# Kernel optimization log

Hardware: AMD Instinct MI355X
Metric: run time of the kernel (lower is better)

## Reference

```python
import jax, jax.numpy as jnp
import numpy as np

B, L, DM, H, DFF = 4, 2048, 512, 8, 2048
D = DM // H            # head dim = 64
FACTOR = 5
U = min(FACTOR * int(np.ceil(np.log(L))), L)  # 40 sampled keys / top-u queries
EPS = 1e-5


def layer_norm(x, g, b):
    m = x.mean(-1, keepdims=True)
    v = ((x - m) ** 2).mean(-1, keepdims=True)
    return (x - m) * jax.lax.rsqrt(v + EPS) * g + b


def setup_inputs() -> dict:
    key = jax.random.key(0)
    ks = jax.random.split(key, 18)
    s = 0.02  # init scale for stability
    return {
        "x": jax.random.normal(ks[0], (B, L, DM), jnp.float32),
        "Wq": jax.random.normal(ks[1], (DM, DM), jnp.float32) * s,
        "bq": jnp.zeros((DM,), jnp.float32),
        "Wk": jax.random.normal(ks[2], (DM, DM), jnp.float32) * s,
        "bk": jnp.zeros((DM,), jnp.float32),
        "Wv": jax.random.normal(ks[3], (DM, DM), jnp.float32) * s,
        "bv": jnp.zeros((DM,), jnp.float32),
        "Wo": jax.random.normal(ks[4], (DM, DM), jnp.float32) * s,
        "bo": jnp.zeros((DM,), jnp.float32),
        "Wc1": jax.random.normal(ks[5], (DFF, DM), jnp.float32) * s,  # conv1d k=1 weight (out,in)
        "bc1": jnp.zeros((DFF,), jnp.float32),
        "Wc2": jax.random.normal(ks[6], (DM, DFF), jnp.float32) * s,
        "bc2": jnp.zeros((DM,), jnp.float32),
        "ln1_g": jnp.ones((DM,), jnp.float32),
        "ln1_b": jnp.zeros((DM,), jnp.float32),
        "ln2_g": jnp.ones((DM,), jnp.float32),
        "ln2_b": jnp.zeros((DM,), jnp.float32),
        "sample_idx": jax.random.randint(ks[7], (L, U), 0, L, jnp.int32),
    }


def reference(x, Wq, bq, Wk, bk, Wv, bv, Wo, bo, Wc1, bc1, Wc2, bc2,
              ln1_g, ln1_b, ln2_g, ln2_b, sample_idx):
    Bb, Ll, _ = x.shape
    # --- AttentionLayer projections -> (B, H, L, D) ---
    q = (x @ Wq + bq).reshape(Bb, Ll, H, D).transpose(0, 2, 1, 3)
    k = (x @ Wk + bk).reshape(Bb, Ll, H, D).transpose(0, 2, 1, 3)
    v = (x @ Wv + bv).reshape(Bb, Ll, H, D).transpose(0, 2, 1, 3)

    # --- ProbSparse: score each query against U sampled keys ---
    K_sample = k[:, :, sample_idx, :]                       # (B,H,L,U,D)
    QK_sample = jnp.einsum('bhld,bhlud->bhlu', q, K_sample)  # (B,H,L,U)
    M = QK_sample.max(-1) - QK_sample.mean(-1)               # sparsity measure (B,H,L)
    _, M_top = jax.lax.top_k(M, U)                           # (B,H,U) top-u query indices

    # --- full attention only for top-u queries ---
    Q_red = jnp.take_along_axis(q, M_top[..., None], axis=2)  # (B,H,U,D)
    scores = jnp.einsum('bhud,bhld->bhul', Q_red, k) / jnp.sqrt(jnp.float32(D))
    attn = jax.nn.softmax(scores, axis=-1)                    # (B,H,U,L)
    ctx_top = jnp.einsum('bhul,bhld->bhud', attn, v)          # (B,H,U,D)

    # --- initial context = mean of V (mask_flag=False); scatter top-u rows ---
    context = jnp.broadcast_to(v.mean(axis=2, keepdims=True), v.shape)
    bi = jnp.arange(Bb)[:, None, None]
    hi = jnp.arange(H)[None, :, None]
    context = context.at[bi, hi, M_top].set(ctx_top)          # (B,H,L,D)

    new_x = context.transpose(0, 2, 1, 3).reshape(Bb, Ll, DM) @ Wo + bo

    # --- residual + norm + conv1d(k=1) FFN + norm ---
    x = layer_norm(x + new_x, ln1_g, ln1_b)
    y = jax.nn.relu(x @ Wc1.T + bc1)
    y = y @ Wc2.T + bc2
    return layer_norm(x + y, ln2_g, ln2_b)
```

## Files before the change

### kernel.cpp

```cpp
#include <hip/hip_runtime.h>
#include <math.h>

static constexpr int Bc = 4, Lc = 2048, DMc = 512, Hc = 8, Dc = 64, DFFc = 2048, Uc = 40;
static constexpr int NT = Bc * Lc;

typedef __attribute__((ext_vector_type(4))) float f32x4;
typedef __attribute__((ext_vector_type(8))) short bf16x8;
typedef unsigned short ushort_t;

__device__ __forceinline__ float wave_sum(float v) {
#pragma unroll
  for (int off = 32; off > 0; off >>= 1) v += __shfl_xor(v, off);
  return v;
}

__device__ __forceinline__ ushort_t f2bf(float f) {
  union { float f; unsigned int u; } c{f};
  unsigned int u = c.u + 0x7fff + ((c.u >> 16) & 1);
  return (ushort_t)(u >> 16);
}

__device__ __forceinline__ unsigned pk2bf(float a, float b) {
  return (unsigned)f2bf(a) | ((unsigned)f2bf(b) << 16);
}

__device__ __forceinline__ void gload16(const ushort_t* g, ushort_t* l) {
  __builtin_amdgcn_global_load_lds(
      (const __attribute__((address_space(1))) unsigned int*)g,
      (__attribute__((address_space(3))) unsigned int*)l, 16, 0, 0);
}

template <int MODE>
__global__ __launch_bounds__(256) void gemm_mfma(
    const ushort_t* __restrict__ A, const ushort_t* __restrict__ Bt,
    const float* __restrict__ bias, float* __restrict__ Cf,
    ushort_t* __restrict__ Cb, float* __restrict__ Qo, float* __restrict__ Ko,
    float* __restrict__ Vo, float* __restrict__ Kt, int M, int N, int K) {
  __shared__ __align__(16) ushort_t As[128 * 32];
  __shared__ __align__(16) ushort_t Bs[128 * 32];
  const int tid = threadIdx.x;
  const int lane = tid & 63, wave = tid >> 6;
  const int m0 = blockIdx.y << 7, n0 = blockIdx.x << 7;
  const int wm = ((wave >> 1) << 6), wn = ((wave & 1) << 6);
  f32x4 acc[4][4] = {};
  const ushort_t* aSrc = A + (size_t)(m0 + (tid >> 2)) * K + ((tid & 3) << 3);
  const ushort_t* bSrc = Bt + (size_t)(n0 + (tid >> 2)) * K + ((tid & 3) << 3);
  ushort_t* aDst = As + wave * 512;
  ushort_t* bDst = Bs + wave * 512;
  const size_t aHalf = (size_t)64 * K, bHalf = (size_t)64 * K;
  for (int k0 = 0; k0 < K; k0 += 32) {
    gload16(aSrc + k0, aDst);
    gload16(aSrc + aHalf + k0, aDst + 2048);
    gload16(bSrc + k0, bDst);
    gload16(bSrc + bHalf + k0, bDst + 2048);
    __syncthreads();
    bf16x8 af[4], bfr[4];
    const int fr = lane & 15, ko = (lane >> 4) << 3;
#pragma unroll
    for (int i = 0; i < 4; ++i) {
      af[i] = *reinterpret_cast<const bf16x8*>(&As[(wm + i * 16 + fr) * 32 + ko]);
      bfr[i] = *reinterpret_cast<const bf16x8*>(&Bs[(wn + i * 16 + fr) * 32 + ko]);
    }
#pragma unroll
    for (int i = 0; i < 4; ++i)
#pragma unroll
      for (int j = 0; j < 4; ++j)
        acc[i][j] = __builtin_amdgcn_mfma_f32_16x16x32_bf16(af[i], bfr[j], acc[i][j], 0, 0, 0);
    __syncthreads();
  }
  const int cr = (lane >> 4) << 2, cc = lane & 15;
#pragma unroll
  for (int j = 0; j < 4; ++j) {
    const int col = n0 + wn + j * 16 + cc;
    const float bsv = bias[col];
#pragma unroll
    for (int i = 0; i < 4; ++i) {
#pragma unroll
      for (int r = 0; r < 4; ++r) {
        const int row = m0 + wm + i * 16 + cr + r;
        float v = acc[i][j][r] + bsv;
        if (MODE == 0) {
          Cf[(size_t)row * N + col] = v;
        } else if (MODE == 1) {
          Cb[(size_t)row * N + col] = f2bf(fmaxf(v, 0.f));
        } else {
          const int which = col >> 9, h = (col >> 6) & 7, d = col & 63;
          const int b = row >> 11, l = row & (Lc - 1);
          const size_t o = ((size_t)(((b << 3) + h) << 11) + l) * 64 + d;
          float* dst = which == 0 ? Qo : (which == 1 ? Ko : Vo);
          dst[o] = v;
          if (which == 1 && Kt)
            Kt[((size_t)(((b << 3) + h) << 6) + d) * Lc + l] = v;
        }
      }
    }
  }
}

__global__ __launch_bounds__(256) void conv_bf16(const float* __restrict__ in,
                                                 ushort_t* __restrict__ out) {
  int i = blockIdx.x * 256 + threadIdx.x;
  float4 v = *reinterpret_cast<const float4*>(&in[(size_t)i * 4]);
  ushort4 o;
  o.x = f2bf(v.x); o.y = f2bf(v.y); o.z = f2bf(v.z); o.w = f2bf(v.w);
  *reinterpret_cast<ushort4*>(&out[(size_t)i * 4]) = o;
}

__global__ __launch_bounds__(256) void tconv(const float* __restrict__ in,
                                             ushort_t* __restrict__ out,
                                             int R, int C, int rowOff) {
  __shared__ float t[32][33];
  const int r0 = blockIdx.y << 5, c0 = blockIdx.x << 5;
  const int tr = threadIdx.x >> 5, tc = threadIdx.x & 31;
#pragma unroll
  for (int p = 0; p < 4; ++p)
    t[tr + p * 8][tc] = in[(size_t)(r0 + tr + p * 8) * C + c0 + tc];
  __syncthreads();
#pragma unroll
  for (int p = 0; p < 4; ++p)
    out[(size_t)(rowOff + c0 + tr + p * 8) * R + r0 + tc] = f2bf(t[tc][tr + p * 8]);
}

__global__ __launch_bounds__(256) void concat_bias(const float* __restrict__ bq,
                                                   const float* __restrict__ bk,
                                                   const float* __restrict__ bv,
                                                   float* __restrict__ o) {
  int i = blockIdx.x * 256 + threadIdx.x;
  o[i] = i < 512 ? bq[i] : (i < 1024 ? bk[i - 512] : bv[i - 1024]);
}

__global__ __launch_bounds__(256) void compute_M_kernel(
    const float* __restrict__ Q, const float* __restrict__ K,
    const int* __restrict__ sidx, float* __restrict__ Mout) {
  const int tid = threadIdx.x;
  const int wave = tid >> 6, lane = tid & 63;
  const int g = lane >> 4, lg = lane & 15;
  const int gw = blockIdx.x * 16 + wave * 4 + g;
  const int bh = gw >> 11, l = gw & (Lc - 1);
  const float4 q4 = *reinterpret_cast<const float4*>(&Q[((size_t)gw << 6) + (lg << 2)]);
  const float* Kbase = K + ((size_t)bh << 17);
  const int* sp = sidx + l * Uc;
  float mx = -1e30f, sm = 0.f;
#pragma unroll 4
  for (int u = 0; u < Uc; ++u) {
    const int idx = sp[u];
    const float4 k4 = *reinterpret_cast<const float4*>(&Kbase[((size_t)idx << 6) + (lg << 2)]);
    float d = q4.x * k4.x + q4.y * k4.y + q4.z * k4.z + q4.w * k4.w;
#pragma unroll
    for (int off = 8; off > 0; off >>= 1) d += __shfl_xor(d, off);
    mx = fmaxf(mx, d);
    sm += d;
  }
  if (lg == 0) Mout[gw] = mx - sm * (1.f / Uc);
}

__global__ __launch_bounds__(256) void topk_kernel(const float* __restrict__ Min,
                                                   int* __restrict__ Mtop) {
  __shared__ float sm[Lc];
  const int bh = blockIdx.x >> 3, chunk = blockIdx.x & 7;
  const int tid = threadIdx.x;
  for (int i = tid; i < Lc; i += 256) sm[i] = Min[bh * Lc + i];
  __syncthreads();
  const int cand = (chunk << 8) + tid;
  const float mv = sm[cand];
  int rank = 0;
  for (int j = 0; j < Lc; j += 4) {
    float4 w4 = *reinterpret_cast<const float4*>(&sm[j]);
    rank += (w4.x > mv || (w4.x == mv && (j + 0) < cand));
    rank += (w4.y > mv || (w4.y == mv && (j + 1) < cand));
    rank += (w4.z > mv || (w4.z == mv && (j + 2) < cand));
    rank += (w4.w > mv || (w4.w == mv && (j + 3) < cand));
  }
  if (rank < Uc) Mtop[bh * Uc + rank] = cand;
}

__global__ __launch_bounds__(256, 3) void attn_flash(
    const float* __restrict__ Q, const float* __restrict__ K,
    const float* __restrict__ V, const int* __restrict__ Mtop,
    float* __restrict__ m_p, float* __restrict__ l_p, float* __restrict__ o_p) {
  __shared__ __align__(16) ushort_t Qs[48 * 80];
  __shared__ __align__(16) ushort_t KVs[128 * 80];
  __shared__ __align__(16) ushort_t Ps[48 * 144];
  __shared__ float mw[4][48];
  __shared__ float lw[4][48];
  const int tid = threadIdx.x;
  const int lane = tid & 63, w = tid >> 6;
  const int cc = lane & 15, hi = lane >> 4;
  const int bh = blockIdx.x >> 4, chunk = blockIdx.x & 15;
  const int kk0 = chunk << 7;
  const float* Qb = Q + ((size_t)bh << 17);
  const float* Kb = K + ((size_t)bh << 17);
  const float* Vb = V + ((size_t)bh << 17);

  for (int i = tid; i < 48 * 16; i += 256) {
    const int r = i >> 4, c4 = (i & 15) << 2;
    uint2 pk{0u, 0u};
    if (r < Uc) {
      const int lsel = Mtop[bh * Uc + r];
      float4 v = *reinterpret_cast<const float4*>(&Qb[((size_t)lsel << 6) + c4]);
      pk.x = pk2bf(v.x, v.y); pk.y = pk2bf(v.z, v.w);
    }
    *reinterpret_cast<uint2*>(&Qs[r * 80 + c4]) = pk;
  }
  for (int i = tid; i < 128 * 16; i += 256) {
    const int r = i >> 4, c4 = (i & 15) << 2;
    float4 v = *reinterpret_cast<const float4*>(&Kb[((size_t)(kk0 + r) << 6) + c4]);
    uint2 pk{pk2bf(v.x, v.y), pk2bf(v.z, v.w)};
    *reinterpret_cast<uint2*>(&KVs[r * 80 + c4]) = pk;
  }
  __syncthreads();

  f32x4 sacc[3][2] = {};
#pragma unroll
  for (int s = 0; s < 2; ++s) {
    bf16x8 af[3], bk[2];
#pragma unroll
    for (int i = 0; i < 3; ++i)
      af[i] = *reinterpret_cast<const bf16x8*>(&Qs[(i * 16 + cc) * 80 + s * 32 + hi * 8]);
#pragma unroll
    for (int jj = 0; jj < 2; ++jj)
      bk[jj] = *reinterpret_cast<const bf16x8*>(&KVs[(w * 32 + jj * 16 + cc) * 80 + s * 32 + hi * 8]);
#pragma unroll
    for (int i = 0; i < 3; ++i)
#pragma unroll
      for (int jj = 0; jj < 2; ++jj)
        sacc[i][jj] = __builtin_amdgcn_mfma_f32_16x16x32_bf16(af[i], bk[jj], sacc[i][jj], 0, 0, 0);
  }

  float mx[3][4];
#pragma unroll
  for (int i = 0; i < 3; ++i)
#pragma unroll
    for (int r = 0; r < 4; ++r)
      mx[i][r] = fmaxf(sacc[i][0][r], sacc[i][1][r]) * 0.125f;
#pragma unroll
  for (int off = 1; off < 16; off <<= 1)
#pragma unroll
    for (int i = 0; i < 3; ++i)
#pragma unroll
      for (int r = 0; r < 4; ++r)
        mx[i][r] = fmaxf(mx[i][r], __shfl_xor(mx[i][r], off));
  if (cc == 0)
#pragma unroll
    for (int i = 0; i < 3; ++i)
#pragma unroll
      for (int r = 0; r < 4; ++r) mw[w][i * 16 + (hi << 2) + r] = mx[i][r];
  __syncthreads();

  float fm[3][4], ls[3][4];
#pragma unroll
  for (int i = 0; i < 3; ++i)
#pragma unroll
    for (int r = 0; r < 4; ++r) {
      const int row = i * 16 + (hi << 2) + r;
      fm[i][r] = fmaxf(fmaxf(mw[0][row], mw[1][row]), fmaxf(mw[2][row], mw[3][row]));
      ls[i][r] = 0.f;
    }
#pragma unroll
  for (int i = 0; i < 3; ++i)
#pragma unroll
    for (int jj = 0; jj < 2; ++jj)
#pragma unroll
      for (int r = 0; r < 4; ++r) {
        float p = __expf(sacc[i][jj][r] * 0.125f - fm[i][r]);
        ls[i][r] += p;
        Ps[(i * 16 + (hi << 2) + r) * 144 + w * 32 + jj * 16 + cc] = f2bf(p);
      }
#pragma unroll
  for (int off = 1; off < 16; off <<= 1)
#pragma unroll
    for (int i = 0; i < 3; ++i)
#pragma unroll
      for (int r = 0; r < 4; ++r) ls[i][r] += __shfl_xor(ls[i][r], off);
  if (cc == 0)
#pragma unroll
    for (int i = 0; i < 3; ++i)
#pragma unroll
      for (int r = 0; r < 4; ++r) lw[w][i * 16 + (hi << 2) + r] = ls[i][r];

  {
    ushort_t* Vt = KVs;
    for (int i = tid; i < 128 * 16; i += 256) {
      const int k = i >> 4, c4 = (i & 15) << 2;
      float4 v = *reinterpret_cast<const float4*>(&Vb[((size_t)(kk0 + k) << 6) + c4]);
      Vt[(c4 + 0) * 144 + k] = f2bf(v.x);
      Vt[(c4 + 1) * 144 + k] = f2bf(v.y);
      Vt[(c4 + 2) * 144 + k] = f2bf(v.z);
      Vt[(c4 + 3) * 144 + k] = f2bf(v.w);
    }
  }
  __syncthreads();

  f32x4 oacc[3] = {};
#pragma unroll
  for (int s = 0; s < 4; ++s) {
    bf16x8 ap[3], bv;
#pragma unroll
    for (int i = 0; i < 3; ++i)
      ap[i] = *reinterpret_cast<const bf16x8*>(&Ps[(i * 16 + cc) * 144 + s * 32 + hi * 8]);
    bv = *reinterpret_cast<const bf16x8*>(&KVs[(w * 16 + cc) * 144 + s * 32 + hi * 8]);
#pragma unroll
    for (int i = 0; i < 3; ++i)
      oacc[i] = __builtin_amdgcn_mfma_f32_16x16x32_bf16(ap[i], bv, oacc[i], 0, 0, 0);
  }
#pragma unroll
  for (int i = 0; i < 3; ++i)
#pragma unroll
    for (int r = 0; r < 4; ++r) {
      const int row = i * 16 + (hi << 2) + r;
      if (row < Uc)
        o_p[((size_t)((bh * Uc + row) * 16 + chunk) << 6) + w * 16 + cc] = oacc[i][r];
    }
  if (w == 0 && cc == 0)
#pragma unroll
    for (int i = 0; i < 3; ++i)
#pragma unroll
      for (int r = 0; r < 4; ++r) {
        const int row = i * 16 + (hi << 2) + r;
        if (row < Uc) {
          m_p[(bh * Uc + row) * 16 + chunk] = fm[i][r];
          l_p[(bh * Uc + row) * 16 + chunk] =
              lw[0][row] + lw[1][row] + lw[2][row] + lw[3][row];
        }
      }
}

__global__ __launch_bounds__(256) void attn_combine(
    const float* __restrict__ m_p, const float* __restrict__ l_p,
    const float* __restrict__ o_p, const int* __restrict__ Mtop,
    ushort_t* __restrict__ ctxb) {
  const int w = (blockIdx.x * 256 + threadIdx.x) >> 6;
  const int lane = threadIdx.x & 63;
  const float* mp = m_p + w * 16;
  const float* lp = l_p + w * 16;
  float M = -1e30f;
#pragma unroll
  for (int c = 0; c < 16; ++c) M = fmaxf(M, mp[c]);
  float denom = 0.f;
  float wgt[16];
#pragma unroll
  for (int c = 0; c < 16; ++c) {
    wgt[c] = __expf(mp[c] - M);
    denom += lp[c] * wgt[c];
  }
  float acc = 0.f;
#pragma unroll
  for (int c = 0; c < 16; ++c)
    acc += o_p[((size_t)w * 16 + c) * 64 + lane] * wgt[c];
  const int bh = w / Uc;
  const int b = bh >> 3, h = bh & 7;
  const int lsel = Mtop[w];
  ctxb[(size_t)(b * Lc + lsel) * DMc + (h << 6) + lane] = f2bf(acc / denom);
}

__global__ __launch_bounds__(64) void vmean_kernel(const float* __restrict__ V,
                                                   float* __restrict__ vmean) {
  int blk = blockIdx.x;
  int bh = blk >> 3, c = blk & 7;
  int lane = threadIdx.x;
  float sm = 0.f;
  int lbase = c << 8;
  for (int l = lbase; l < lbase + 256; ++l)
    sm += V[((size_t)(bh * Lc + l) << 6) + lane];
  atomicAdd(&vmean[(bh << 6) + lane], sm * (1.f / Lc));
}

__global__ __launch_bounds__(256) void build_ctx_kernel(const float* __restrict__ vmean,
                                                        ushort_t* __restrict__ ctxb) {
  int idx = blockIdx.x * 256 + threadIdx.x;
  ctxb[idx] = f2bf(vmean[((idx >> 20) << 9) + (idx & 511)]);
}

__global__ __launch_bounds__(256) void add_ln_kernel(
    const float* __restrict__ resid, const float* __restrict__ yin,
    const float* __restrict__ g, const float* __restrict__ bbias,
    float* __restrict__ out, ushort_t* __restrict__ outb) {
  __shared__ float vals[DMc];
  __shared__ float red[4];
  int row = blockIdx.x, tid = threadIdx.x;
  size_t base = (size_t)row * DMc;
  float lsum = 0.f;
  for (int c = tid; c < DMc; c += 256) {
    float t = resid[base + c] + yin[base + c];
    vals[c] = t;
    lsum += t;
  }
  lsum = wave_sum(lsum);
  if ((tid & 63) == 0) red[tid >> 6] = lsum;
  __syncthreads();
  float mean = (red[0] + red[1] + red[2] + red[3]) * (1.f / DMc);
  __syncthreads();
  float lv = 0.f;
  for (int c = tid; c < DMc; c += 256) {
    float dv = vals[c] - mean;
    lv += dv * dv;
  }
  lv = wave_sum(lv);
  if ((tid & 63) == 0) red[tid >> 6] = lv;
  __syncthreads();
  float inv = rsqrtf((red[0] + red[1] + red[2] + red[3]) * (1.f / DMc) + 1e-5f);
  for (int c = tid; c < DMc; c += 256) {
    float o = (vals[c] - mean) * inv * g[c] + bbias[c];
    out[base + c] = o;
    if (outb) outb[base + c] = f2bf(o);
  }
}

extern "C" void kernel_launch(void* const* d_in, const int* in_sizes, int n_in,
                              void* d_out, int out_size, void* d_ws, size_t ws_size,
                              hipStream_t stream) {
  (void)in_sizes; (void)n_in; (void)out_size; (void)ws_size;
  const float* x   = (const float*)d_in[0];
  const float* Wq  = (const float*)d_in[1];
  const float* bq  = (const float*)d_in[2];
  const float* Wk  = (const float*)d_in[3];
  const float* bk  = (const float*)d_in[4];
  const float* Wv  = (const float*)d_in[5];
  const float* bv  = (const float*)d_in[6];
  const float* Wo  = (const float*)d_in[7];
  const float* bo  = (const float*)d_in[8];
  const float* Wc1 = (const float*)d_in[9];
  const float* bc1 = (const float*)d_in[10];
  const float* Wc2 = (const float*)d_in[11];
  const float* bc2 = (const float*)d_in[12];
  const float* g1  = (const float*)d_in[13];
  const float* b1  = (const float*)d_in[14];
  const float* g2  = (const float*)d_in[15];
  const float* b2  = (const float*)d_in[16];
  const int* sidx  = (const int*)d_in[17];
  float* out = (float*)d_out;

  float* ws = (float*)d_ws;
  float* Qb     = ws;
  float* Kb     = ws + 4194304;
  float* Vb     = ws + 8388608;
  float* m_p    = ws + 12582912;
  float* l_p    = ws + 12603392;
  float* o_p    = ws + 12623872;
  float* X1     = ws + 16777216;
  ushort_t* xb   = (ushort_t*)(ws + 20971520);
  ushort_t* Wqkvt= (ushort_t*)(ws + 23068672);
  ushort_t* Wot  = (ushort_t*)(ws + 23461888);
  ushort_t* Wc1b = (ushort_t*)(ws + 23592960);
  ushort_t* Wc2b = (ushort_t*)(ws + 24117248);
  float* bqkv   = ws + 24641536;
  float* Mb     = ws + 24643072;
  float* vmean  = ws + 24708608;
  int* Mtop     = (int*)(ws + 24710656);
  ushort_t* CTXb = (ushort_t*)Vb;
  ushort_t* X1b  = (ushort_t*)(ws + 12582912);
  ushort_t* Yb   = (ushort_t*)Qb;

  dim3 blk(256);
  conv_bf16<<<4096, blk, 0, stream>>>(x, xb);
  tconv<<<dim3(16, 16), blk, 0, stream>>>(Wq, Wqkvt, 512, 512, 0);
  tconv<<<dim3(16, 16), blk, 0, stream>>>(Wk, Wqkvt, 512, 512, 512);
  tconv<<<dim3(16, 16), blk, 0, stream>>>(Wv, Wqkvt, 512, 512, 1024);
  tconv<<<dim3(16, 16), blk, 0, stream>>>(Wo, Wot, 512, 512, 0);
  conv_bf16<<<1024, blk, 0, stream>>>(Wc1, Wc1b);
  conv_bf16<<<1024, blk, 0, stream>>>(Wc2, Wc2b);
  concat_bias<<<6, blk, 0, stream>>>(bq, bk, bv, bqkv);

  gemm_mfma<2><<<dim3(12, 64), blk, 0, stream>>>(xb, Wqkvt, bqkv, nullptr, nullptr,
                                                 Qb, Kb, Vb, nullptr, NT, 1536, DMc);
  compute_M_kernel<<<4096, blk, 0, stream>>>(Qb, Kb, sidx, Mb);
  topk_kernel<<<256, blk, 0, stream>>>(Mb, Mtop);
  attn_flash<<<512, blk, 0, stream>>>(Qb, Kb, Vb, Mtop, m_p, l_p, o_p);
  hipMemsetAsync(vmean, 0, Bc * Hc * Dc * sizeof(float), stream);
  vmean_kernel<<<Bc * Hc * 8, dim3(64), 0, stream>>>(Vb, vmean);
  build_ctx_kernel<<<16384, blk, 0, stream>>>(vmean, CTXb);
  attn_combine<<<320, blk, 0, stream>>>(m_p, l_p, o_p, Mtop, CTXb);

  gemm_mfma<0><<<dim3(4, 64), blk, 0, stream>>>(CTXb, Wot, bo, out, nullptr,
                                                nullptr, nullptr, nullptr, nullptr,
                                                NT, DMc, DMc);
  add_ln_kernel<<<NT, blk, 0, stream>>>(x, out, g1, b1, X1, X1b);
  gemm_mfma<1><<<dim3(16, 64), blk, 0, stream>>>(X1b, Wc1b, bc1, nullptr, Yb,
                                                 nullptr, nullptr, nullptr, nullptr,
                                                 NT, DFFc, DMc);
  gemm_mfma<0><<<dim3(4, 64), blk, 0, stream>>>(Yb, Wc2b, bc2, out, nullptr,
                                                nullptr, nullptr, nullptr, nullptr,
                                                NT, DMc, DFFc);
  add_ln_kernel<<<NT, blk, 0, stream>>>(X1, out, g2, b2, out, nullptr);
}
```

Before: 408.9 us.

## Store Q/K/V projections in bf16 and swizzle GEMM/M-kernel blocks across XCDs

The QKV projection GEMM now writes Q, K and V as bf16 instead of fp32, and drops the unused transposed-K output. The M-score, attention and V-mean kernels read bf16 directly. This halves the traffic for writing and re-reading the projections and removes per-load conversion in the attention kernel. The GEMM and compute_M kernels also remap block indices so neighbouring tiles or heads land on the same XCD for better L2 locality. The cost is that Q and K are rounded to bf16 before the sparsity measure, which may change the top-u query selection on near-ties.

```diff
diff --git a/kernel.cpp b/kernel.cpp
--- a/kernel.cpp
+++ b/kernel.cpp
@@ -20,8 +20,9 @@
   return (ushort_t)(u >> 16);
 }
 
-__device__ __forceinline__ unsigned pk2bf(float a, float b) {
-  return (unsigned)f2bf(a) | ((unsigned)f2bf(b) << 16);
+__device__ __forceinline__ float bf2f(ushort_t b) {
+  union { unsigned int u; float f; } c{(unsigned int)b << 16};
+  return c.f;
 }
 
 __device__ __forceinline__ void gload16(const ushort_t* g, ushort_t* l) {
@@ -34,13 +35,16 @@
 __global__ __launch_bounds__(256) void gemm_mfma(
     const ushort_t* __restrict__ A, const ushort_t* __restrict__ Bt,
     const float* __restrict__ bias, float* __restrict__ Cf,
-    ushort_t* __restrict__ Cb, float* __restrict__ Qo, float* __restrict__ Ko,
-    float* __restrict__ Vo, float* __restrict__ Kt, int M, int N, int K) {
+    ushort_t* __restrict__ Cb, ushort_t* __restrict__ Qo, ushort_t* __restrict__ Ko,
+    ushort_t* __restrict__ Vo, int M, int N, int K) {
   __shared__ __align__(16) ushort_t As[128 * 32];
   __shared__ __align__(16) ushort_t Bs[128 * 32];
   const int tid = threadIdx.x;
   const int lane = tid & 63, wave = tid >> 6;
-  const int m0 = blockIdx.y << 7, n0 = blockIdx.x << 7;
+  const int nwg = gridDim.x * gridDim.y;
+  const int lin = blockIdx.y * gridDim.x + blockIdx.x;
+  const int swz = (lin & 7) * (nwg >> 3) + (lin >> 3);
+  const int m0 = (swz / gridDim.x) << 7, n0 = (swz % gridDim.x) << 7;
   const int wm = ((wave >> 1) << 6), wn = ((wave & 1) << 6);
   f32x4 acc[4][4] = {};
   const ushort_t* aSrc = A + (size_t)(m0 + (tid >> 2)) * K + ((tid & 3) << 3);
@@ -87,10 +91,8 @@
           const int which = col >> 9, h = (col >> 6) & 7, d = col & 63;
           const int b = row >> 11, l = row & (Lc - 1);
           const size_t o = ((size_t)(((b << 3) + h) << 11) + l) * 64 + d;
-          float* dst = which == 0 ? Qo : (which == 1 ? Ko : Vo);
-          dst[o] = v;
-          if (which == 1 && Kt)
-            Kt[((size_t)(((b << 3) + h) << 6) + d) * Lc + l] = v;
+          ushort_t* dst = which == 0 ? Qo : (which == 1 ? Ko : Vo);
+          dst[o] = f2bf(v);
         }
       }
     }
@@ -130,22 +132,27 @@
 }
 
 __global__ __launch_bounds__(256) void compute_M_kernel(
-    const float* __restrict__ Q, const float* __restrict__ K,
+    const ushort_t* __restrict__ Q, const ushort_t* __restrict__ K,
     const int* __restrict__ sidx, float* __restrict__ Mout) {
   const int tid = threadIdx.x;
   const int wave = tid >> 6, lane = tid & 63;
   const int g = lane >> 4, lg = lane & 15;
-  const int gw = blockIdx.x * 16 + wave * 4 + g;
-  const int bh = gw >> 11, l = gw & (Lc - 1);
-  const float4 q4 = *reinterpret_cast<const float4*>(&Q[((size_t)gw << 6) + (lg << 2)]);
-  const float* Kbase = K + ((size_t)bh << 17);
+  const int p = blockIdx.x;
+  const int xcd = p & 7, j = p >> 3;
+  const int bh = xcd + ((j >> 7) << 3);
+  const int inner = j & 127;
+  const int gw = (bh << 11) + (inner << 4) + wave * 4 + g;
+  const int l = gw & (Lc - 1);
+  const ushort4 q4 = *reinterpret_cast<const ushort4*>(&Q[((size_t)gw << 6) + (lg << 2)]);
+  const float qx = bf2f(q4.x), qy = bf2f(q4.y), qz = bf2f(q4.z), qw = bf2f(q4.w);
+  const ushort_t* Kbase = K + ((size_t)bh << 17);
   const int* sp = sidx + l * Uc;
   float mx = -1e30f, sm = 0.f;
 #pragma unroll 4
   for (int u = 0; u < Uc; ++u) {
     const int idx = sp[u];
-    const float4 k4 = *reinterpret_cast<const float4*>(&Kbase[((size_t)idx << 6) + (lg << 2)]);
-    float d = q4.x * k4.x + q4.y * k4.y + q4.z * k4.z + q4.w * k4.w;
+    const ushort4 k4 = *reinterpret_cast<const ushort4*>(&Kbase[((size_t)idx << 6) + (lg << 2)]);
+    float d = qx * bf2f(k4.x) + qy * bf2f(k4.y) + qz * bf2f(k4.z) + qw * bf2f(k4.w);
 #pragma unroll
     for (int off = 8; off > 0; off >>= 1) d += __shfl_xor(d, off);
     mx = fmaxf(mx, d);
@@ -175,8 +182,8 @@
 }
 
 __global__ __launch_bounds__(256, 3) void attn_flash(
-    const float* __restrict__ Q, const float* __restrict__ K,
-    const float* __restrict__ V, const int* __restrict__ Mtop,
+    const ushort_t* __restrict__ Q, const ushort_t* __restrict__ K,
+    const ushort_t* __restrict__ V, const int* __restrict__ Mtop,
     float* __restrict__ m_p, float* __restrict__ l_p, float* __restrict__ o_p) {
   __shared__ __align__(16) ushort_t Qs[48 * 80];
   __shared__ __align__(16) ushort_t KVs[128 * 80];
@@ -188,25 +195,23 @@
   const int cc = lane & 15, hi = lane >> 4;
   const int bh = blockIdx.x >> 4, chunk = blockIdx.x & 15;
   const int kk0 = chunk << 7;
-  const float* Qb = Q + ((size_t)bh << 17);
-  const float* Kb = K + ((size_t)bh << 17);
-  const float* Vb = V + ((size_t)bh << 17);
-
-  for (int i = tid; i < 48 * 16; i += 256) {
-    const int r = i >> 4, c4 = (i & 15) << 2;
-    uint2 pk{0u, 0u};
+  const ushort_t* Qb = Q + ((size_t)bh << 17);
+  const ushort_t* Kb = K + ((size_t)bh << 17);
+  const ushort_t* Vb = V + ((size_t)bh << 17);
+
+  for (int i = tid; i < 48 * 8; i += 256) {
+    const int r = i >> 3, c8 = (i & 7) << 3;
+    bf16x8 v = 0;
     if (r < Uc) {
       const int lsel = Mtop[bh * Uc + r];
-      float4 v = *reinterpret_cast<const float4*>(&Qb[((size_t)lsel << 6) + c4]);
-      pk.x = pk2bf(v.x, v.y); pk.y = pk2bf(v.z, v.w);
-    }
-    *reinterpret_cast<uint2*>(&Qs[r * 80 + c4]) = pk;
-  }
-  for (int i = tid; i < 128 * 16; i += 256) {
-    const int r = i >> 4, c4 = (i & 15) << 2;
-    float4 v = *reinterpret_cast<const float4*>(&Kb[((size_t)(kk0 + r) << 6) + c4]);
-    uint2 pk{pk2bf(v.x, v.y), pk2bf(v.z, v.w)};
-    *reinterpret_cast<uint2*>(&KVs[r * 80 + c4]) = pk;
+      v = *reinterpret_cast<const bf16x8*>(&Qb[((size_t)lsel << 6) + c8]);
+    }
+    *reinterpret_cast<bf16x8*>(&Qs[r * 80 + c8]) = v;
+  }
+  for (int i = tid; i < 128 * 8; i += 256) {
+    const int r = i >> 3, c8 = (i & 7) << 3;
+    *reinterpret_cast<bf16x8*>(&KVs[r * 80 + c8]) =
+        *reinterpret_cast<const bf16x8*>(&Kb[((size_t)(kk0 + r) << 6) + c8]);
   }
   __syncthreads();
 
@@ -280,13 +285,11 @@
 
   {
     ushort_t* Vt = KVs;
-    for (int i = tid; i < 128 * 16; i += 256) {
-      const int k = i >> 4, c4 = (i & 15) << 2;
-      float4 v = *reinterpret_cast<const float4*>(&Vb[((size_t)(kk0 + k) << 6) + c4]);
-      Vt[(c4 + 0) * 144 + k] = f2bf(v.x);
-      Vt[(c4 + 1) * 144 + k] = f2bf(v.y);
-      Vt[(c4 + 2) * 144 + k] = f2bf(v.z);
-      Vt[(c4 + 3) * 144 + k] = f2bf(v.w);
+    for (int i = tid; i < 128 * 8; i += 256) {
+      const int k = i >> 3, c8 = (i & 7) << 3;
+      bf16x8 v = *reinterpret_cast<const bf16x8*>(&Vb[((size_t)(kk0 + k) << 6) + c8]);
+#pragma unroll
+      for (int jq = 0; jq < 8; ++jq) Vt[(c8 + jq) * 144 + k] = (ushort_t)v[jq];
     }
   }
   __syncthreads();
@@ -353,7 +356,7 @@
   ctxb[(size_t)(b * Lc + lsel) * DMc + (h << 6) + lane] = f2bf(acc / denom);
 }
 
-__global__ __launch_bounds__(64) void vmean_kernel(const float* __restrict__ V,
+__global__ __launch_bounds__(64) void vmean_kernel(const ushort_t* __restrict__ V,
                                                    float* __restrict__ vmean) {
   int blk = blockIdx.x;
   int bh = blk >> 3, c = blk & 7;
@@ -361,7 +364,7 @@
   float sm = 0.f;
   int lbase = c << 8;
   for (int l = lbase; l < lbase + 256; ++l)
-    sm += V[((size_t)(bh * Lc + l) << 6) + lane];
+    sm += bf2f(V[((size_t)(bh * Lc + l) << 6) + lane]);
   atomicAdd(&vmean[(bh << 6) + lane], sm * (1.f / Lc));
 }
 
@@ -431,9 +434,9 @@
   float* out = (float*)d_out;
 
   float* ws = (float*)d_ws;
-  float* Qb     = ws;
-  float* Kb     = ws + 4194304;
-  float* Vb     = ws + 8388608;
+  ushort_t* Qb   = (ushort_t*)ws;
+  ushort_t* Kb   = (ushort_t*)(ws + 4194304);
+  ushort_t* Vb   = (ushort_t*)(ws + 8388608);
   float* m_p    = ws + 12582912;
   float* l_p    = ws + 12603392;
   float* o_p    = ws + 12623872;
@@ -447,9 +450,9 @@
   float* Mb     = ws + 24643072;
   float* vmean  = ws + 24708608;
   int* Mtop     = (int*)(ws + 24710656);
-  ushort_t* CTXb = (ushort_t*)Vb;
+  ushort_t* CTXb = Vb;
   ushort_t* X1b  = (ushort_t*)(ws + 12582912);
-  ushort_t* Yb   = (ushort_t*)Qb;
+  ushort_t* Yb   = (ushort_t*)ws;
 
   dim3 blk(256);
   conv_bf16<<<4096, blk, 0, stream>>>(x, xb);
@@ -462,7 +465,7 @@
   concat_bias<<<6, blk, 0, stream>>>(bq, bk, bv, bqkv);
 
   gemm_mfma<2><<<dim3(12, 64), blk, 0, stream>>>(xb, Wqkvt, bqkv, nullptr, nullptr,
-                                                 Qb, Kb, Vb, nullptr, NT, 1536, DMc);
+                                                 Qb, Kb, Vb, NT, 1536, DMc);
   compute_M_kernel<<<4096, blk, 0, stream>>>(Qb, Kb, sidx, Mb);
   topk_kernel<<<256, blk, 0, stream>>>(Mb, Mtop);
   attn_flash<<<512, blk, 0, stream>>>(Qb, Kb, Vb, Mtop, m_p, l_p, o_p);
@@ -472,14 +475,14 @@
   attn_combine<<<320, blk, 0, stream>>>(m_p, l_p, o_p, Mtop, CTXb);
 
   gemm_mfma<0><<<dim3(4, 64), blk, 0, stream>>>(CTXb, Wot, bo, out, nullptr,
-                                                nullptr, nullptr, nullptr, nullptr,
+                                                nullptr, nullptr, nullptr,
                                                 NT, DMc, DMc);
   add_ln_kernel<<<NT, blk, 0, stream>>>(x, out, g1, b1, X1, X1b);
   gemm_mfma<1><<<dim3(16, 64), blk, 0, stream>>>(X1b, Wc1b, bc1, nullptr, Yb,
-                                                 nullptr, nullptr, nullptr, nullptr,
+                                                 nullptr, nullptr, nullptr,
                                                  NT, DFFc, DMc);
   gemm_mfma<0><<<dim3(4, 64), blk, 0, stream>>>(Yb, Wc2b, bc2, out, nullptr,
-                                                nullptr, nullptr, nullptr, nullptr,
+                                                nullptr, nullptr, nullptr,
                                                 NT, DMc, DFFc);
   add_ln_kernel<<<NT, blk, 0, stream>>>(X1, out, g2, b2, out, nullptr);
 }
```

After: 382.0 us. -6.6%, faster.
